# Performance work log

Hardware: AMD Instinct MI355X
Metric: run time of the kernel (lower is better)

Reference implementation:

```python
import jax, jax.numpy as jnp
import numpy as np

SA_LAMBDA = 1.0
IC_LAMBDA = 1.0
EPS = 1e-12  # torch F.normalize eps


def setup_inputs() -> dict:
    key = jax.random.key(0)
    k1, k2, k3, k4 = jax.random.split(key, 4)
    TF = jax.random.normal(k1, (16, 512, 32, 32), dtype=jnp.float32)
    SF = jax.random.normal(k2, (16, 512, 32, 32), dtype=jnp.float32)
    t_out = jax.random.normal(k3, (16, 21, 128, 128), dtype=jnp.float32)
    s_out = jax.random.normal(k4, (16, 21, 128, 128), dtype=jnp.float32)
    return {"TF": TF, "SF": SF, "t_out": t_out, "s_out": s_out}


def _l2_normalize_last(A):
    # matches torch.nn.functional.normalize(x, dim=2): x / max(||x||, eps)
    n = jnp.linalg.norm(A, axis=-1, keepdims=True)
    return A / jnp.maximum(n, EPS)


def _channel_weighted_spatial_gram(F4):
    # Algebraic fusion of einsum('bij,bki->bijk') + einsum('bijk,bi->bjk'):
    # ATT[b,m,n] = sum_c F[b,c,m] * F[b,c,n] * Fc[b,c]
    b, c, h, w = F4.shape
    Fc = jnp.sum(jnp.abs(F4), axis=(2, 3))          # [b, c]
    Fm = F4.reshape(b, c, h * w)                     # [b, c, M]
    A = jnp.einsum('bcm,bc,bcn->bmn', Fm, Fc, Fm)    # [b, M, M]
    return _l2_normalize_last(A)


def _normalized_channel_gram(L):
    # ICC[b,i,j] = sum_m L[b,i,m] * L[b,j,m], then L2-normalize along last dim
    G = jnp.einsum('bim,bjm->bij', L, L)
    return _l2_normalize_last(G)


def reference(TF, SF, t_out, s_out):
    b, c, h, w = TF.shape
    M = h * w
    ATT_T = _channel_weighted_spatial_gram(TF)
    ATT_S = _channel_weighted_spatial_gram(SF)
    diff = ATT_S - ATT_T
    SA_loss = SA_LAMBDA * jnp.sum(diff * diff) / (b * M ** 2)

    bb, cc, hh, ww = s_out.shape
    s_logit = s_out.reshape(bb, cc, hh * ww)
    t_logit = t_out.reshape(bb, cc, hh * ww)
    G_diff = _normalized_channel_gram(s_logit) - _normalized_channel_gram(t_logit)
    ic_loss = IC_LAMBDA * jnp.sum(G_diff * G_diff) / (cc * bb)

    return (s_out, ic_loss, SA_loss)
```

## Files before the change

kernel.cpp:

```cpp
#include <hip/hip_runtime.h>
#include <hip/hip_bf16.h>
#include <cstdint>
#include <cstddef>

typedef __bf16 bf16x8 __attribute__((ext_vector_type(8)));
typedef float f32x4 __attribute__((ext_vector_type(4)));

__device__ __forceinline__ void gload_lds16(const void* g, void* l) {
  __builtin_amdgcn_global_load_lds((const __attribute__((address_space(1))) void*)g,
                                   (__attribute__((address_space(3))) void*)l, 16, 0, 0);
}

__global__ void fc_kernel(const float* __restrict__ TF, const float* __restrict__ SF,
                          float* __restrict__ sqrtFc) {
  int wv = threadIdx.x >> 6, lane = threadIdx.x & 63;
  int row = blockIdx.x * 4 + wv;
  const float* X = (row < 8192) ? TF : SF;
  const float* p = X + (size_t)(row & 8191) * 1024;
  float s = 0.f;
#pragma unroll
  for (int it = 0; it < 4; ++it) {
    float4 v = *reinterpret_cast<const float4*>(p + (size_t)(it * 64 + lane) * 4);
    s += fabsf(v.x) + fabsf(v.y) + fabsf(v.z) + fabsf(v.w);
  }
#pragma unroll
  for (int m = 32; m; m >>= 1) s += __shfl_xor(s, m);
  if (lane == 0) sqrtFc[row] = sqrtf(s);
}

__global__ void wprep_kernel(const float* __restrict__ TF, const float* __restrict__ SF,
                             const float* __restrict__ sqrtFc,
                             __hip_bfloat16* __restrict__ Wt, __hip_bfloat16* __restrict__ Ws) {
  __shared__ float lds[32][33];
  int z = blockIdx.z;
  int t = z >> 4, b = z & 15;
  int m0 = blockIdx.x * 32, c0 = blockIdx.y * 32;
  const float* X = ((t ? SF : TF) + (size_t)b * 512 * 1024);
  __hip_bfloat16* W = ((t ? Ws : Wt) + (size_t)b * 1024 * 512);
  int tr = threadIdx.x >> 5, tc = threadIdx.x & 31;
#pragma unroll
  for (int i = 0; i < 4; ++i) {
    int r = i * 8 + tr;
    lds[r][tc] = X[(size_t)(c0 + r) * 1024 + m0 + tc];
  }
  __syncthreads();
  float scale = sqrtFc[t * 8192 + b * 512 + c0 + tc];
#pragma unroll
  for (int i = 0; i < 4; ++i) {
    int m = i * 8 + tr;
    W[(size_t)(m0 + m) * 512 + (c0 + tc)] = __float2bfloat16(lds[tc][m] * scale);
  }
}

__device__ __forceinline__ void syrk_tile(const __hip_bfloat16* __restrict__ Wb,
                                          __hip_bfloat16* As, __hip_bfloat16* Bs,
                                          int tm, int tn, f32x4 (&acc)[4][4]) {
  const int tid = threadIdx.x;
  const int lane = tid & 63, wv = tid >> 6;
  const int wr = wv >> 1, wc = wv & 1;
  const int g = lane >> 4, c0 = lane & 15;
  const __hip_bfloat16* Bsrc = (tm == tn) ? As : Bs;
  for (int kt = 0; kt < 8; ++kt) {
#pragma unroll
    for (int i = 0; i < 4; ++i) {
      int ci = i * 256 + tid;
      int row = ci >> 3, ch = ci & 7;
      int wbase = (i * 256 + wv * 64) * 8;
      gload_lds16(Wb + (size_t)(tm * 128 + row) * 512 + kt * 64 + ch * 8, As + wbase);
      if (tm != tn)
        gload_lds16(Wb + (size_t)(tn * 128 + row) * 512 + kt * 64 + ch * 8, Bs + wbase);
    }
    __syncthreads();
#pragma unroll
    for (int kk = 0; kk < 2; ++kk) {
      bf16x8 a[4], bb[4];
#pragma unroll
      for (int mi = 0; mi < 4; ++mi)
        a[mi] = *reinterpret_cast<const bf16x8*>(As + (size_t)(wr * 64 + mi * 16 + c0) * 64 + kk * 32 + g * 8);
#pragma unroll
      for (int ni = 0; ni < 4; ++ni)
        bb[ni] = *reinterpret_cast<const bf16x8*>(Bsrc + (size_t)(wc * 64 + ni * 16 + c0) * 64 + kk * 32 + g * 8);
#pragma unroll
      for (int mi = 0; mi < 4; ++mi)
#pragma unroll
        for (int ni = 0; ni < 4; ++ni)
          acc[mi][ni] = __builtin_amdgcn_mfma_f32_16x16x32_bf16(a[mi], bb[ni], acc[mi][ni], 0, 0, 0);
    }
    __syncthreads();
  }
}

__global__ void __launch_bounds__(256, 2) syrk_fused_kernel(
    const __hip_bfloat16* __restrict__ Wt, const __hip_bfloat16* __restrict__ Ws,
    float* __restrict__ nT, float* __restrict__ nS, float* __restrict__ cross) {
  __shared__ __hip_bfloat16 As[128 * 64], Bs[128 * 64];
  int b = blockIdx.z;
  int bx = blockIdx.x, tm = 0;
  while (bx >= 8 - tm) { bx -= 8 - tm; tm++; }
  int tn = tm + bx;
  f32x4 accT[4][4], accS[4][4];
#pragma unroll
  for (int mi = 0; mi < 4; ++mi)
#pragma unroll
    for (int ni = 0; ni < 4; ++ni) {
      accT[mi][ni] = (f32x4){0.f, 0.f, 0.f, 0.f};
      accS[mi][ni] = (f32x4){0.f, 0.f, 0.f, 0.f};
    }
  syrk_tile(Wt + (size_t)b * 524288, As, Bs, tm, tn, accT);
  syrk_tile(Ws + (size_t)b * 524288, As, Bs, tm, tn, accS);

  int lane = threadIdx.x & 63, wv = threadIdx.x >> 6;
  int wr = wv >> 1, wc = wv & 1, g = lane >> 4, c0 = lane & 15;
  float* pT = nT + (size_t)b * 1024;
  float* pS = nS + (size_t)b * 1024;
  float* pC = cross + (size_t)b * 1024;
#pragma unroll
  for (int mi = 0; mi < 4; ++mi)
#pragma unroll
    for (int r = 0; r < 4; ++r) {
      float sT = 0.f, sS = 0.f, sC = 0.f;
#pragma unroll
      for (int ni = 0; ni < 4; ++ni) {
        float tv = accT[mi][ni][r], sv = accS[mi][ni][r];
        sT += tv * tv; sS += sv * sv; sC += tv * sv;
      }
#pragma unroll
      for (int msk = 1; msk < 16; msk <<= 1) {
        sT += __shfl_xor(sT, msk); sS += __shfl_xor(sS, msk); sC += __shfl_xor(sC, msk);
      }
      if (c0 == 0) {
        int m = tm * 128 + wr * 64 + mi * 16 + g * 4 + r;
        atomicAdd(pT + m, sT); atomicAdd(pS + m, sS); atomicAdd(pC + m, sC);
      }
    }
  if (tm != tn) {
#pragma unroll
    for (int ni = 0; ni < 4; ++ni) {
      float sT = 0.f, sS = 0.f, sC = 0.f;
#pragma unroll
      for (int mi = 0; mi < 4; ++mi)
#pragma unroll
        for (int r = 0; r < 4; ++r) {
          float tv = accT[mi][ni][r], sv = accS[mi][ni][r];
          sT += tv * tv; sS += sv * sv; sC += tv * sv;
        }
      sT += __shfl_xor(sT, 16); sS += __shfl_xor(sS, 16); sC += __shfl_xor(sC, 16);
      sT += __shfl_xor(sT, 32); sS += __shfl_xor(sS, 32); sC += __shfl_xor(sC, 32);
      if (g == 0) {
        int n = tn * 128 + wc * 64 + ni * 16 + c0;
        atomicAdd(pT + n, sT); atomicAdd(pS + n, sS); atomicAdd(pC + n, sC);
      }
    }
  }
}

__global__ void icgram2_kernel(const float* __restrict__ t_out, const float* __restrict__ s_out,
                               float* __restrict__ G) {
  __shared__ float lds[22 * 516];
  int chunk = blockIdx.x;
  int z = blockIdx.y;
  int t = z >> 4, bb = z & 15;
  const float* L = (t ? s_out : t_out) + (size_t)bb * 21 * 16384 + (size_t)chunk * 512;
  int tid = threadIdx.x;
  for (int idx = tid; idx < 22 * 128; idx += 264) {
    int r = idx >> 7, c = idx & 127;
    float4 v;
    if (r < 21) v = *reinterpret_cast<const float4*>(L + (size_t)r * 16384 + c * 4);
    else { v.x = 0.f; v.y = 0.f; v.z = 0.f; v.w = 0.f; }
    *reinterpret_cast<float4*>(&lds[r * 516 + c * 4]) = v;
  }
  __syncthreads();
  int ms = tid & 3, pb = tid >> 2;
  int p = pb, gi = 0;
  while (p >= 11 - gi) { p -= 11 - gi; gi++; }
  int gj = gi + p;
  const float* ri0 = &lds[(2 * gi) * 516 + ms * 128];
  const float* ri1 = ri0 + 516;
  const float* rj0 = &lds[(2 * gj) * 516 + ms * 128];
  const float* rj1 = rj0 + 516;
  float a00 = 0.f, a01 = 0.f, a10 = 0.f, a11 = 0.f;
#pragma unroll
  for (int mi = 0; mi < 32; ++mi) {
    float4 va0 = *reinterpret_cast<const float4*>(ri0 + mi * 4);
    float4 va1 = *reinterpret_cast<const float4*>(ri1 + mi * 4);
    float4 vb0 = *reinterpret_cast<const float4*>(rj0 + mi * 4);
    float4 vb1 = *reinterpret_cast<const float4*>(rj1 + mi * 4);
    a00 += va0.x * vb0.x + va0.y * vb0.y + va0.z * vb0.z + va0.w * vb0.w;
    a01 += va0.x * vb1.x + va0.y * vb1.y + va0.z * vb1.z + va0.w * vb1.w;
    a10 += va1.x * vb0.x + va1.y * vb0.y + va1.z * vb0.z + va1.w * vb0.w;
    a11 += va1.x * vb1.x + va1.y * vb1.y + va1.z * vb1.z + va1.w * vb1.w;
  }
  a00 += __shfl_xor(a00, 1); a00 += __shfl_xor(a00, 2);
  a01 += __shfl_xor(a01, 1); a01 += __shfl_xor(a01, 2);
  a10 += __shfl_xor(a10, 1); a10 += __shfl_xor(a10, 2);
  a11 += __shfl_xor(a11, 1); a11 += __shfl_xor(a11, 2);
  if (ms == 0) {
    float* Gz = G + (size_t)z * 441;
    int i0 = 2 * gi, i1 = i0 + 1, j0 = 2 * gj, j1 = j0 + 1;
    atomicAdd(&Gz[i0 * 21 + j0], a00);
    if (j1 < 21) atomicAdd(&Gz[i0 * 21 + j1], a01);
    if (i1 < 21 && gi != gj) atomicAdd(&Gz[i1 * 21 + j0], a10);
    if (i1 < 21 && j1 < 21) atomicAdd(&Gz[i1 * 21 + j1], a11);
  }
}

__global__ void finalize_kernel(const float* __restrict__ G, const float* __restrict__ nT,
                                const float* __restrict__ nS, const float* __restrict__ cross,
                                float* __restrict__ out2) {
  __shared__ float red[8];
  int tid = threadIdx.x;
  float sa = 0.f;
  for (int idx = tid; idx < 16384; idx += 512) {
    float a = nT[idx], s = nS[idx], c = cross[idx];
    float NT = fmaxf(sqrtf(a), 1e-12f), NS = fmaxf(sqrtf(s), 1e-12f);
    sa += a / (NT * NT) + s / (NS * NS) - 2.f * c / (NT * NS);
  }
  float ic = 0.f;
  if (tid < 336) {
    int b = tid / 21, i = tid % 21;
    const float* gt = G + (size_t)b * 441;
    const float* gs = G + (size_t)(16 + b) * 441;
    float nt = 0.f, ns = 0.f;
    for (int j = 0; j < 21; ++j) {
      int idx2 = (i <= j) ? i * 21 + j : j * 21 + i;
      float vt = gt[idx2], vs = gs[idx2];
      nt += vt * vt; ns += vs * vs;
    }
    float rt = 1.f / fmaxf(sqrtf(nt), 1e-12f);
    float rs = 1.f / fmaxf(sqrtf(ns), 1e-12f);
    for (int j = 0; j < 21; ++j) {
      int idx2 = (i <= j) ? i * 21 + j : j * 21 + i;
      float d = gs[idx2] * rs - gt[idx2] * rt;
      ic += d * d;
    }
  }
  int lane = tid & 63, wv = tid >> 6;
#pragma unroll
  for (int m = 32; m; m >>= 1) { sa += __shfl_xor(sa, m); ic += __shfl_xor(ic, m); }
  if (lane == 0) red[wv] = sa;
  __syncthreads();
  if (tid == 0) { float s = 0.f; for (int w = 0; w < 8; ++w) s += red[w]; out2[1] = s * (1.0f / 16777216.0f); }
  __syncthreads();
  if (lane == 0) red[wv] = ic;
  __syncthreads();
  if (tid == 0) { float s = 0.f; for (int w = 0; w < 8; ++w) s += red[w]; out2[0] = s * (1.0f / 336.0f); }
}

extern "C" void kernel_launch(void* const* d_in, const int* in_sizes, int n_in,
                              void* d_out, int out_size, void* d_ws, size_t ws_size,
                              hipStream_t stream) {
  const float* TF = (const float*)d_in[0];
  const float* SF = (const float*)d_in[1];
  const float* t_out = (const float*)d_in[2];
  const float* s_out = (const float*)d_in[3];
  float* out = (float*)d_out;
  char* ws = (char*)d_ws;

  float* nT = (float*)(ws + 0);
  float* nS = (float*)(ws + 65536);
  float* cross = (float*)(ws + 131072);
  float* G = (float*)(ws + 196608);
  float* sqrtFc = (float*)(ws + 253184);
  __hip_bfloat16* Wt = (__hip_bfloat16*)(ws + 318720);
  __hip_bfloat16* Ws = (__hip_bfloat16*)(ws + 318720 + 16777216);

  hipMemcpyAsync(d_out, (const void*)s_out, (size_t)5505024 * 4, hipMemcpyDeviceToDevice, stream);
  hipMemsetAsync(ws, 0, 253056, stream);

  fc_kernel<<<4096, 256, 0, stream>>>(TF, SF, sqrtFc);
  wprep_kernel<<<dim3(32, 16, 32), 256, 0, stream>>>(TF, SF, sqrtFc, Wt, Ws);
  syrk_fused_kernel<<<dim3(36, 1, 16), 256, 0, stream>>>(Wt, Ws, nT, nS, cross);
  icgram2_kernel<<<dim3(32, 32), 264, 0, stream>>>(t_out, s_out, G);
  finalize_kernel<<<1, 512, 0, stream>>>(G, nT, nS, cross, out + 5505024);
}
```

Before: 152.7 us.

## Fuse abs-sum into bf16 prep, double-buffer and swizzle SYRK, vectorize finalize

Merges the channel abs-sum kernel and the transpose/scale kernel into one prep kernel that stages 16 channel rows in LDS, computes the sqrt scale, and writes packed 32-byte bf16 rows. This removes one full read of TF/SF and a launch. The SYRK kernel now runs the T and S passes as a single 16-step loop with double-buffered LDS loads, an XOR-swizzled LDS layout to reduce bank conflicts, and a 1D grid remapped so blocks spread across batches. Finalize uses 1024 threads with float4 loads. The costs are more LDS per block (about 66KB in prep, 64KB in SYRK), which may lower occupancy.

```diff
diff --git a/kernel.cpp b/kernel.cpp
--- a/kernel.cpp
+++ b/kernel.cpp
@@ -11,93 +11,89 @@
                                    (__attribute__((address_space(3))) void*)l, 16, 0, 0);
 }
 
-__global__ void fc_kernel(const float* __restrict__ TF, const float* __restrict__ SF,
-                          float* __restrict__ sqrtFc) {
-  int wv = threadIdx.x >> 6, lane = threadIdx.x & 63;
-  int row = blockIdx.x * 4 + wv;
-  const float* X = (row < 8192) ? TF : SF;
-  const float* p = X + (size_t)(row & 8191) * 1024;
-  float s = 0.f;
-#pragma unroll
-  for (int it = 0; it < 4; ++it) {
-    float4 v = *reinterpret_cast<const float4*>(p + (size_t)(it * 64 + lane) * 4);
-    s += fabsf(v.x) + fabsf(v.y) + fabsf(v.z) + fabsf(v.w);
-  }
-#pragma unroll
-  for (int m = 32; m; m >>= 1) s += __shfl_xor(s, m);
-  if (lane == 0) sqrtFc[row] = sqrtf(s);
-}
-
-__global__ void wprep_kernel(const float* __restrict__ TF, const float* __restrict__ SF,
-                             const float* __restrict__ sqrtFc,
-                             __hip_bfloat16* __restrict__ Wt, __hip_bfloat16* __restrict__ Ws) {
-  __shared__ float lds[32][33];
-  int z = blockIdx.z;
-  int t = z >> 4, b = z & 15;
-  int m0 = blockIdx.x * 32, c0 = blockIdx.y * 32;
-  const float* X = ((t ? SF : TF) + (size_t)b * 512 * 1024);
-  __hip_bfloat16* W = ((t ? Ws : Wt) + (size_t)b * 1024 * 512);
-  int tr = threadIdx.x >> 5, tc = threadIdx.x & 31;
+__global__ void __launch_bounds__(256) prep_kernel(const float* __restrict__ TF,
+                                                   const float* __restrict__ SF,
+                                                   __hip_bfloat16* __restrict__ Wt,
+                                                   __hip_bfloat16* __restrict__ Ws) {
+  __shared__ float Xs[16 * 1028];
+  __shared__ float partial[4][16];
+  __shared__ float scale[16];
+  int id = blockIdx.x;
+  int t = id >> 9, b = (id >> 5) & 15, cb = id & 31;
+  const float* Xg = (t ? SF : TF) + ((size_t)b * 512 + (size_t)cb * 16) * 1024;
+  __hip_bfloat16* W = (t ? Ws : Wt) + (size_t)b * 524288 + cb * 16;
+  int tid = threadIdx.x;
+#pragma unroll
+  for (int it = 0; it < 16; ++it)
+    *reinterpret_cast<float4*>(&Xs[it * 1028 + tid * 4]) =
+        *reinterpret_cast<const float4*>(Xg + (size_t)it * 1024 + tid * 4);
+  __syncthreads();
+  {
+    int r = tid & 15, seg = tid >> 4;
+    float s = 0.f;
+#pragma unroll
+    for (int i = 0; i < 16; ++i) {
+      float4 v = *reinterpret_cast<const float4*>(&Xs[r * 1028 + seg * 64 + i * 4]);
+      s += fabsf(v.x) + fabsf(v.y) + fabsf(v.z) + fabsf(v.w);
+    }
+    s += __shfl_xor(s, 16); s += __shfl_xor(s, 32);
+    if ((tid & 63) < 16) partial[tid >> 6][tid & 15] = s;
+    __syncthreads();
+    if (tid < 16) scale[tid] = sqrtf(partial[0][tid] + partial[1][tid] + partial[2][tid] + partial[3][tid]);
+    __syncthreads();
+  }
+  float sc[16];
+#pragma unroll
+  for (int c = 0; c < 16; ++c) sc[c] = scale[c];
+#pragma unroll
+  for (int j = 0; j < 4; ++j) {
+    int m = j * 256 + tid;
+    union { __hip_bfloat16 h[16]; uint4 u[2]; } pk;
+#pragma unroll
+    for (int c = 0; c < 16; ++c) pk.h[c] = __float2bfloat16(Xs[c * 1028 + m] * sc[c]);
+    uint4* dst = reinterpret_cast<uint4*>(W + (size_t)m * 512);
+    dst[0] = pk.u[0];
+    dst[1] = pk.u[1];
+  }
+}
+
+__device__ __forceinline__ void stage_tile(const __hip_bfloat16* __restrict__ Wm,
+                                           const __hip_bfloat16* __restrict__ Wn,
+                                           __hip_bfloat16* As, __hip_bfloat16* Bs,
+                                           int kt, bool diag) {
+  int tid = threadIdx.x, wv = tid >> 6;
 #pragma unroll
   for (int i = 0; i < 4; ++i) {
-    int r = i * 8 + tr;
-    lds[r][tc] = X[(size_t)(c0 + r) * 1024 + m0 + tc];
-  }
-  __syncthreads();
-  float scale = sqrtFc[t * 8192 + b * 512 + c0 + tc];
-#pragma unroll
-  for (int i = 0; i < 4; ++i) {
-    int m = i * 8 + tr;
-    W[(size_t)(m0 + m) * 512 + (c0 + tc)] = __float2bfloat16(lds[tc][m] * scale);
-  }
-}
-
-__device__ __forceinline__ void syrk_tile(const __hip_bfloat16* __restrict__ Wb,
-                                          __hip_bfloat16* As, __hip_bfloat16* Bs,
-                                          int tm, int tn, f32x4 (&acc)[4][4]) {
+    int ci = i * 256 + tid;
+    int row = ci >> 3, slot = ci & 7;
+    int gslot = slot ^ (row & 7);
+    int wbase = (i * 256 + wv * 64) * 8;
+    gload_lds16(Wm + (size_t)row * 512 + kt * 64 + gslot * 8, As + wbase);
+    if (!diag)
+      gload_lds16(Wn + (size_t)row * 512 + kt * 64 + gslot * 8, Bs + wbase);
+  }
+}
+
+__global__ void __launch_bounds__(256, 2) syrk_fused_kernel(
+    const __hip_bfloat16* __restrict__ Wt, const __hip_bfloat16* __restrict__ Ws,
+    float* __restrict__ nT, float* __restrict__ nS, float* __restrict__ cross) {
+  __shared__ __hip_bfloat16 As[2][128 * 64], Bs[2][128 * 64];
+  int lid = blockIdx.x;
+  int swz = (lid & 7) * 72 + (lid >> 3);
+  int b = swz / 36, tilec = swz % 36;
+  int bx = tilec, tm = 0;
+  while (bx >= 8 - tm) { bx -= 8 - tm; ++tm; }
+  int tn = tm + bx;
+  bool diag = (tm == tn);
+  const __hip_bfloat16* WT = Wt + (size_t)b * 524288;
+  const __hip_bfloat16* WS = Ws + (size_t)b * 524288;
+
   const int tid = threadIdx.x;
   const int lane = tid & 63, wv = tid >> 6;
   const int wr = wv >> 1, wc = wv & 1;
   const int g = lane >> 4, c0 = lane & 15;
-  const __hip_bfloat16* Bsrc = (tm == tn) ? As : Bs;
-  for (int kt = 0; kt < 8; ++kt) {
-#pragma unroll
-    for (int i = 0; i < 4; ++i) {
-      int ci = i * 256 + tid;
-      int row = ci >> 3, ch = ci & 7;
-      int wbase = (i * 256 + wv * 64) * 8;
-      gload_lds16(Wb + (size_t)(tm * 128 + row) * 512 + kt * 64 + ch * 8, As + wbase);
-      if (tm != tn)
-        gload_lds16(Wb + (size_t)(tn * 128 + row) * 512 + kt * 64 + ch * 8, Bs + wbase);
-    }
-    __syncthreads();
-#pragma unroll
-    for (int kk = 0; kk < 2; ++kk) {
-      bf16x8 a[4], bb[4];
-#pragma unroll
-      for (int mi = 0; mi < 4; ++mi)
-        a[mi] = *reinterpret_cast<const bf16x8*>(As + (size_t)(wr * 64 + mi * 16 + c0) * 64 + kk * 32 + g * 8);
-#pragma unroll
-      for (int ni = 0; ni < 4; ++ni)
-        bb[ni] = *reinterpret_cast<const bf16x8*>(Bsrc + (size_t)(wc * 64 + ni * 16 + c0) * 64 + kk * 32 + g * 8);
-#pragma unroll
-      for (int mi = 0; mi < 4; ++mi)
-#pragma unroll
-        for (int ni = 0; ni < 4; ++ni)
-          acc[mi][ni] = __builtin_amdgcn_mfma_f32_16x16x32_bf16(a[mi], bb[ni], acc[mi][ni], 0, 0, 0);
-    }
-    __syncthreads();
-  }
-}
-
-__global__ void __launch_bounds__(256, 2) syrk_fused_kernel(
-    const __hip_bfloat16* __restrict__ Wt, const __hip_bfloat16* __restrict__ Ws,
-    float* __restrict__ nT, float* __restrict__ nS, float* __restrict__ cross) {
-  __shared__ __hip_bfloat16 As[128 * 64], Bs[128 * 64];
-  int b = blockIdx.z;
-  int bx = blockIdx.x, tm = 0;
-  while (bx >= 8 - tm) { bx -= 8 - tm; tm++; }
-  int tn = tm + bx;
+  const int rx = c0 & 7;
+
   f32x4 accT[4][4], accS[4][4];
 #pragma unroll
   for (int mi = 0; mi < 4; ++mi)
@@ -106,11 +102,48 @@
       accT[mi][ni] = (f32x4){0.f, 0.f, 0.f, 0.f};
       accS[mi][ni] = (f32x4){0.f, 0.f, 0.f, 0.f};
     }
-  syrk_tile(Wt + (size_t)b * 524288, As, Bs, tm, tn, accT);
-  syrk_tile(Ws + (size_t)b * 524288, As, Bs, tm, tn, accS);
-
-  int lane = threadIdx.x & 63, wv = threadIdx.x >> 6;
-  int wr = wv >> 1, wc = wv & 1, g = lane >> 4, c0 = lane & 15;
+
+  stage_tile(WT + (size_t)tm * 65536, WT + (size_t)tn * 65536, As[0], Bs[0], 0, diag);
+  __syncthreads();
+
+  for (int s = 0; s < 16; ++s) {
+    int cur = s & 1;
+    if (s < 15) {
+      int s1 = s + 1;
+      const __hip_bfloat16* base = (s1 < 8) ? WT : WS;
+      stage_tile(base + (size_t)tm * 65536, base + (size_t)tn * 65536,
+                 As[cur ^ 1], Bs[cur ^ 1], s1 & 7, diag);
+    }
+    const __hip_bfloat16* Asb = As[cur];
+    const __hip_bfloat16* Bsb = diag ? As[cur] : Bs[cur];
+    bool isT = (s < 8);
+#pragma unroll
+    for (int kk = 0; kk < 2; ++kk) {
+      int chunk = ((kk * 4 + g) ^ rx) * 8;
+      bf16x8 a[4], bb[4];
+#pragma unroll
+      for (int mi = 0; mi < 4; ++mi)
+        a[mi] = *reinterpret_cast<const bf16x8*>(Asb + (wr * 64 + mi * 16 + c0) * 64 + chunk);
+#pragma unroll
+      for (int ni = 0; ni < 4; ++ni)
+        bb[ni] = *reinterpret_cast<const bf16x8*>(Bsb + (wc * 64 + ni * 16 + c0) * 64 + chunk);
+      if (isT) {
+#pragma unroll
+        for (int mi = 0; mi < 4; ++mi)
+#pragma unroll
+          for (int ni = 0; ni < 4; ++ni)
+            accT[mi][ni] = __builtin_amdgcn_mfma_f32_16x16x32_bf16(a[mi], bb[ni], accT[mi][ni], 0, 0, 0);
+      } else {
+#pragma unroll
+        for (int mi = 0; mi < 4; ++mi)
+#pragma unroll
+          for (int ni = 0; ni < 4; ++ni)
+            accS[mi][ni] = __builtin_amdgcn_mfma_f32_16x16x32_bf16(a[mi], bb[ni], accS[mi][ni], 0, 0, 0);
+      }
+    }
+    __syncthreads();
+  }
+
   float* pT = nT + (size_t)b * 1024;
   float* pS = nS + (size_t)b * 1024;
   float* pC = cross + (size_t)b * 1024;
@@ -133,7 +166,7 @@
         atomicAdd(pT + m, sT); atomicAdd(pS + m, sS); atomicAdd(pC + m, sC);
       }
     }
-  if (tm != tn) {
+  if (!diag) {
 #pragma unroll
     for (int ni = 0; ni < 4; ++ni) {
       float sT = 0.f, sS = 0.f, sC = 0.f;
@@ -207,13 +240,21 @@
 __global__ void finalize_kernel(const float* __restrict__ G, const float* __restrict__ nT,
                                 const float* __restrict__ nS, const float* __restrict__ cross,
                                 float* __restrict__ out2) {
-  __shared__ float red[8];
+  __shared__ float red[16];
   int tid = threadIdx.x;
   float sa = 0.f;
-  for (int idx = tid; idx < 16384; idx += 512) {
-    float a = nT[idx], s = nS[idx], c = cross[idx];
-    float NT = fmaxf(sqrtf(a), 1e-12f), NS = fmaxf(sqrtf(s), 1e-12f);
-    sa += a / (NT * NT) + s / (NS * NS) - 2.f * c / (NT * NS);
+#pragma unroll
+  for (int it = 0; it < 4; ++it) {
+    int i4 = it * 1024 + tid;
+    float4 a = reinterpret_cast<const float4*>(nT)[i4];
+    float4 s4 = reinterpret_cast<const float4*>(nS)[i4];
+    float4 c4 = reinterpret_cast<const float4*>(cross)[i4];
+#pragma unroll
+    for (int k = 0; k < 4; ++k) {
+      float a1 = (&a.x)[k], s1 = (&s4.x)[k], c1 = (&c4.x)[k];
+      float NT = fmaxf(sqrtf(a1), 1e-12f), NS = fmaxf(sqrtf(s1), 1e-12f);
+      sa += a1 / (NT * NT) + s1 / (NS * NS) - 2.f * c1 / (NT * NS);
+    }
   }
   float ic = 0.f;
   if (tid < 336) {
@@ -239,11 +280,11 @@
   for (int m = 32; m; m >>= 1) { sa += __shfl_xor(sa, m); ic += __shfl_xor(ic, m); }
   if (lane == 0) red[wv] = sa;
   __syncthreads();
-  if (tid == 0) { float s = 0.f; for (int w = 0; w < 8; ++w) s += red[w]; out2[1] = s * (1.0f / 16777216.0f); }
+  if (tid == 0) { float s = 0.f; for (int w = 0; w < 16; ++w) s += red[w]; out2[1] = s * (1.0f / 16777216.0f); }
   __syncthreads();
   if (lane == 0) red[wv] = ic;
   __syncthreads();
-  if (tid == 0) { float s = 0.f; for (int w = 0; w < 8; ++w) s += red[w]; out2[0] = s * (1.0f / 336.0f); }
+  if (tid == 0) { float s = 0.f; for (int w = 0; w < 16; ++w) s += red[w]; out2[0] = s * (1.0f / 336.0f); }
 }
 
 extern "C" void kernel_launch(void* const* d_in, const int* in_sizes, int n_in,
@@ -260,16 +301,14 @@
   float* nS = (float*)(ws + 65536);
   float* cross = (float*)(ws + 131072);
   float* G = (float*)(ws + 196608);
-  float* sqrtFc = (float*)(ws + 253184);
-  __hip_bfloat16* Wt = (__hip_bfloat16*)(ws + 318720);
-  __hip_bfloat16* Ws = (__hip_bfloat16*)(ws + 318720 + 16777216);
+  __hip_bfloat16* Wt = (__hip_bfloat16*)(ws + 262144);
+  __hip_bfloat16* Ws = (__hip_bfloat16*)(ws + 262144 + 16777216);
 
   hipMemcpyAsync(d_out, (const void*)s_out, (size_t)5505024 * 4, hipMemcpyDeviceToDevice, stream);
   hipMemsetAsync(ws, 0, 253056, stream);
 
-  fc_kernel<<<4096, 256, 0, stream>>>(TF, SF, sqrtFc);
-  wprep_kernel<<<dim3(32, 16, 32), 256, 0, stream>>>(TF, SF, sqrtFc, Wt, Ws);
-  syrk_fused_kernel<<<dim3(36, 1, 16), 256, 0, stream>>>(Wt, Ws, nT, nS, cross);
+  prep_kernel<<<1024, 256, 0, stream>>>(TF, SF, Wt, Ws);
+  syrk_fused_kernel<<<576, 256, 0, stream>>>(Wt, Ws, nT, nS, cross);
   icgram2_kernel<<<dim3(32, 32), 264, 0, stream>>>(t_out, s_out, G);
-  finalize_kernel<<<1, 512, 0, stream>>>(G, nT, nS, cross, out + 5505024);
-}
+  finalize_kernel<<<1, 1024, 0, stream>>>(G, nT, nS, cross, out + 5505024);
+}
```

After: 125.8 us. 1.21x faster.
